# Kernel optimization log

Hardware: AMD Instinct MI355X
Metric: run time of the kernel (lower is better)

The kernel has to match this reference:

```python
import jax, jax.numpy as jnp
import numpy as np

D_MODEL = 1024
NUM_HEADS = 16
D_K = D_MODEL // NUM_HEADS
B, S = 2, 2048


def setup_inputs() -> dict:
    key = jax.random.key(0)
    ks = jax.random.split(key, 11)
    sc = 1.0 / np.sqrt(D_MODEL)
    return {
        "Q_input": jax.random.normal(ks[0], (B, S, D_MODEL), jnp.float32),
        "K_input": jax.random.normal(ks[1], (B, S, D_MODEL), jnp.float32),
        "V_input": jax.random.normal(ks[2], (B, S, D_MODEL), jnp.float32),
        "Wq": jax.random.normal(ks[3], (D_MODEL, D_MODEL), jnp.float32) * sc,
        "bq": jax.random.normal(ks[4], (D_MODEL,), jnp.float32) * 0.01,
        "Wk": jax.random.normal(ks[5], (D_MODEL, D_MODEL), jnp.float32) * sc,
        "bk": jax.random.normal(ks[6], (D_MODEL,), jnp.float32) * 0.01,
        "Wv": jax.random.normal(ks[7], (D_MODEL, D_MODEL), jnp.float32) * sc,
        "bv": jax.random.normal(ks[8], (D_MODEL,), jnp.float32) * 0.01,
        "Wo": jax.random.normal(ks[9], (D_MODEL, D_MODEL), jnp.float32) * sc,
        "bo": jax.random.normal(ks[10], (D_MODEL,), jnp.float32) * 0.01,
    }


def reference(Q_input, K_input, V_input, Wq, bq, Wk, bk, Wv, bv, Wo, bo):
    # Linear projections (torch Linear: x @ W.T + b)
    Q = Q_input @ Wq.T + bq  # [B,S,D]
    K = K_input @ Wk.T + bk
    V = V_input @ Wv.T + bv
    # split heads -> [B,H,S,dk]
    def split(x):
        return x.reshape(B, S, NUM_HEADS, D_K).transpose(0, 2, 1, 3)
    Qh, Kh, Vh = split(Q), split(K), split(V)
    scale = 1.0 / jnp.sqrt(jnp.asarray(D_K, Qh.dtype))
    scores = jnp.einsum('bhqd,bhkd->bhqk', Qh, Kh) * scale  # [B,H,S,S]
    attn = jax.nn.softmax(scores, axis=-1)
    ctx = jnp.einsum('bhqk,bhkd->bhqd', attn, Vh)  # [B,H,S,dk]
    concat = ctx.transpose(0, 2, 1, 3).reshape(B, S, D_MODEL)
    out = concat @ Wo.T + bo  # dropout is identity in eval
    return out
```

## Files before the change

kernel.cpp:

```cpp
#include <hip/hip_runtime.h>
#include <stdint.h>

#define DM   1024
#define NH   16
#define DKH  64
#define BBATCH 2
#define SEQ  2048
#define MTOK (BBATCH*SEQ)

typedef unsigned short u16;
typedef unsigned int   u32;
typedef __attribute__((ext_vector_type(8))) short  bf16x8;
typedef __attribute__((ext_vector_type(4))) float  f32x4;

struct PtrArr11 { const void* p[11]; };
struct U16Arr11 { u16* p[11]; };

__device__ __forceinline__ float bf2f(u16 u) {
  union { unsigned int i; float f; } z; z.i = ((unsigned int)u) << 16; return z.f;
}
__device__ __forceinline__ u16 f2bf(float f) {
  union { float f; unsigned int i; } z; z.f = f;
  unsigned int i = z.i + 0x7fffu + ((z.i >> 16) & 1u);
  return (u16)(i >> 16);
}

__device__ __forceinline__ bf16x8 u4_to_bf(u32 a, u32 b, u32 c, u32 d) {
  union { u32 u[4]; bf16x8 v; } z; z.u[0] = a; z.u[1] = b; z.u[2] = c; z.u[3] = d; return z.v;
}

__device__ __forceinline__ void gld16(const void* g, void* l) {
  __builtin_amdgcn_global_load_lds(
      (const __attribute__((address_space(1))) void*)g,
      (__attribute__((address_space(3))) void*)l,
      16, 0, 0);
}

__global__ void k_detect(const unsigned int* __restrict__ w, int* __restrict__ flag) {
  const int ln = threadIdx.x & 63;
  const unsigned int word = w[ln];
  const unsigned int ex = (word >> 7) & 0xFFu;
  const int hit = (ex >= 100u && ex <= 126u) ? 1 : 0;
  unsigned long long m = __ballot(hit);
  if (ln == 0) *flag = (__popcll(m) >= 40) ? 0 : 1;
}

__global__ __launch_bounds__(256) void k_convert_all(PtrArr11 src, U16Arr11 dst,
                                                     const int* __restrict__ flag) {
  if (*flag == 0) return;
  const int b = blockIdx.x;
  int seg, base;
  if      (b <  2048) { seg = 0;  base = 0;    }
  else if (b <  4096) { seg = 1;  base = 2048; }
  else if (b <  6144) { seg = 2;  base = 4096; }
  else if (b <  6656) { seg = 3;  base = 6144; }
  else if (b == 6656) { seg = 4;  base = 6656; }
  else if (b <  7169) { seg = 5;  base = 6657; }
  else if (b == 7169) { seg = 6;  base = 7169; }
  else if (b <  7682) { seg = 7;  base = 7170; }
  else if (b == 7682) { seg = 8;  base = 7682; }
  else if (b <  8195) { seg = 9;  base = 7683; }
  else                { seg = 10; base = 8195; }
  const int n = (seg < 3) ? (MTOK * DM) : ((seg & 1) ? (DM * DM) : DM);
  const int i0 = (b - base) * 2048 + threadIdx.x * 8;
  if (i0 >= n) return;
  const float* s = (const float*)src.p[seg] + i0;
  const f32x4 x0 = *(const f32x4*)(s);
  const f32x4 x1 = *(const f32x4*)(s + 4);
  bf16x8 o;
#pragma unroll
  for (int j = 0; j < 4; ++j) o[j] = (short)f2bf(x0[j]);
#pragma unroll
  for (int j = 0; j < 4; ++j) o[4 + j] = (short)f2bf(x1[j]);
  *(bf16x8*)(dst.p[seg] + i0) = o;
}

__device__ __forceinline__ void gemm_body64(const u16* __restrict__ X,
                                            const u16* __restrict__ W,
                                            const u16* __restrict__ bias,
                                            void* __restrict__ out,
                                            int isf32out)
{
  __shared__ __attribute__((aligned(16))) u16 sA[128 * 64];
  __shared__ __attribute__((aligned(16))) u16 sB[128 * 64];
  const int tid = threadIdx.x;
  const int ln = tid & 63, wv = tid >> 6;
  const int wm = wv & 1, wn = wv >> 1;
  const int m0 = blockIdx.y * 128, n0 = blockIdx.x * 128;
  const int fr = ln & 15, fq = ln >> 4;
  const int fr7 = fr & 7;
  const int srow = ln >> 3;
  const int scol = ((ln & 7) ^ srow) * 8;

  f32x4 acc[4][4];
#pragma unroll
  for (int i = 0; i < 4; ++i)
#pragma unroll
    for (int j = 0; j < 4; ++j) acc[i][j] = (f32x4){0.f, 0.f, 0.f, 0.f};

  const u16* pA = X + (size_t)(m0 + wv * 32 + srow) * DM + scol;
  const u16* pB = W + (size_t)(n0 + wv * 32 + srow) * DM + scol;
  u16* lA = sA + wv * 32 * 64;
  u16* lB = sB + wv * 32 * 64;

  for (int k0 = 0; k0 < DM; k0 += 64) {
#pragma unroll
    for (int c = 0; c < 4; ++c) {
      gld16(pA + (size_t)(c * 8) * DM + k0, lA + c * 8 * 64);
      gld16(pB + (size_t)(c * 8) * DM + k0, lB + c * 8 * 64);
    }
    asm volatile("s_waitcnt vmcnt(0)" ::: "memory");
    __syncthreads();

    bf16x8 af[4][2], bfg[4][2];
#pragma unroll
    for (int t = 0; t < 4; ++t)
#pragma unroll
      for (int ks = 0; ks < 2; ++ks) {
        af[t][ks]  = *(const bf16x8*)(sA + (wm * 64 + t * 16 + fr) * 64 + ((ks * 4 + fq) ^ fr7) * 8);
        bfg[t][ks] = *(const bf16x8*)(sB + (wn * 64 + t * 16 + fr) * 64 + ((ks * 4 + fq) ^ fr7) * 8);
      }
#pragma unroll
    for (int i = 0; i < 4; ++i)
#pragma unroll
      for (int j = 0; j < 4; ++j) {
        acc[i][j] = __builtin_amdgcn_mfma_f32_16x16x32_bf16(af[i][0], bfg[j][0], acc[i][j], 0, 0, 0);
        acc[i][j] = __builtin_amdgcn_mfma_f32_16x16x32_bf16(af[i][1], bfg[j][1], acc[i][j], 0, 0, 0);
      }
    __syncthreads();
  }

#pragma unroll
  for (int i = 0; i < 4; ++i) {
    const int row = m0 + wm * 64 + i * 16 + fq * 4;
#pragma unroll
    for (int j = 0; j < 4; ++j) {
      const int col = n0 + wn * 64 + j * 16 + fr;
      const float bv = bf2f(bias[col]);
#pragma unroll
      for (int r = 0; r < 4; ++r) {
        const float val = acc[i][j][r] + bv;
        const size_t idx = (size_t)(row + r) * DM + col;
        if (isf32out) ((float*)out)[idx] = val;
        else          ((u16*)out)[idx]   = f2bf(val);
      }
    }
  }
}

__device__ __forceinline__ void gemm_body_n64(const u16* __restrict__ X,
                                              const u16* __restrict__ W,
                                              const u16* __restrict__ bias,
                                              void* __restrict__ out,
                                              int isf32out)
{
  __shared__ __attribute__((aligned(16))) u16 sA[128 * 32];
  __shared__ __attribute__((aligned(16))) u16 sB[64 * 32];
  const int tid = threadIdx.x;
  const int ln = tid & 63, wv = tid >> 6;
  const int wm = wv >> 1, wn = wv & 1;
  const int m0 = blockIdx.y * 128, n0 = blockIdx.x * 64;
  const int fr = ln & 15, fq = ln >> 4;
  const int srow = ln >> 2, sslot = (ln & 3) * 8;

  f32x4 acc[4][2];
#pragma unroll
  for (int i = 0; i < 4; ++i)
#pragma unroll
    for (int j = 0; j < 2; ++j) acc[i][j] = (f32x4){0.f, 0.f, 0.f, 0.f};

  const u16* pA = X + (size_t)(m0 + wv * 32 + srow) * DM + sslot;
  const u16* pB = W + (size_t)(n0 + wv * 16 + srow) * DM + sslot;
  u16* lA0 = sA + (wv * 2) * 512; u16* lA1 = sA + (wv * 2 + 1) * 512;
  u16* lB  = sB + wv * 512;

  for (int k0 = 0; k0 < DM; k0 += 32) {
    gld16(pA + k0,           lA0);
    gld16(pA + 16 * DM + k0, lA1);
    gld16(pB + k0,           lB);
    asm volatile("s_waitcnt vmcnt(0)" ::: "memory");
    __syncthreads();

    bf16x8 af[4], bfg[2];
#pragma unroll
    for (int t = 0; t < 4; ++t)
      af[t]  = *(const bf16x8*)(sA + (wm * 64 + t * 16 + fr) * 32 + fq * 8);
#pragma unroll
    for (int t = 0; t < 2; ++t)
      bfg[t] = *(const bf16x8*)(sB + (wn * 32 + t * 16 + fr) * 32 + fq * 8);
#pragma unroll
    for (int i = 0; i < 4; ++i)
#pragma unroll
      for (int j = 0; j < 2; ++j)
        acc[i][j] = __builtin_amdgcn_mfma_f32_16x16x32_bf16(af[i], bfg[j], acc[i][j], 0, 0, 0);
    __syncthreads();
  }

#pragma unroll
  for (int i = 0; i < 4; ++i) {
    const int row = m0 + wm * 64 + i * 16 + fq * 4;
#pragma unroll
    for (int j = 0; j < 2; ++j) {
      const int col = n0 + wn * 32 + j * 16 + fr;
      const float bv = bf2f(bias[col]);
#pragma unroll
      for (int r = 0; r < 4; ++r) {
        const float val = acc[i][j][r] + bv;
        const size_t idx = (size_t)(row + r) * DM + col;
        if (isf32out) ((float*)out)[idx] = val;
        else          ((u16*)out)[idx]   = f2bf(val);
      }
    }
  }
}

__global__ __launch_bounds__(256, 2) void k_gemm_qkv(
    PtrArr11 orig, U16Arr11 conv, const int* __restrict__ flag,
    u16* oq, u16* ok, u16* ov)
{
  const int f = *flag;
  const int z = blockIdx.z;
  const u16* X  = f ? conv.p[z]         : (const u16*)orig.p[z];
  const u16* W  = f ? conv.p[3 + 2 * z] : (const u16*)orig.p[3 + 2 * z];
  const u16* bi = f ? conv.p[4 + 2 * z] : (const u16*)orig.p[4 + 2 * z];
  u16* o = (z == 0) ? oq : (z == 1) ? ok : ov;
  gemm_body64(X, W, bi, o, 0);
}

__global__ __launch_bounds__(256, 2) void k_gemm_one(
    const u16* X, const void* Wo_o, const u16* Wo_c,
    const void* bo_o, const u16* bo_c, const int* __restrict__ flag, void* o)
{
  const int f = *flag;
  const u16* W  = f ? Wo_c : (const u16*)Wo_o;
  const u16* bi = f ? bo_c : (const u16*)bo_o;
  gemm_body_n64(X, W, bi, o, f);
}

__global__ __launch_bounds__(256) void k_transpose(const u16* __restrict__ in,
                                                   u16* __restrict__ out)
{
  __shared__ u16 t[64][66];
  const int b = blockIdx.z;
  const int s0 = blockIdx.x * 64, d0 = blockIdx.y * 64;
  const int c = threadIdx.x & 63, r0 = threadIdx.x >> 6;
#pragma unroll
  for (int i = 0; i < 16; ++i) {
    const int r = r0 + 4 * i;
    t[r][c] = in[(size_t)(b * SEQ + s0 + r) * DM + d0 + c];
  }
  __syncthreads();
#pragma unroll
  for (int i = 0; i < 16; ++i) {
    const int r = r0 + 4 * i;
    out[(size_t)(b * DM + d0 + r) * SEQ + s0 + c] = t[c][r];
  }
}

__global__ __launch_bounds__(256, 2) void k_attn(
    const u16* __restrict__ Qp, const u16* __restrict__ Kp,
    const u16* __restrict__ Vt, u16* __restrict__ ctx)
{
  __shared__ __attribute__((aligned(16))) u16 sK[2][64 * 64];
  __shared__ __attribute__((aligned(16))) u16 sV[2][64 * 64];

  const int tid = threadIdx.x;
  const int ln = tid & 63, wv = tid >> 6;
  const int bh = blockIdx.y;
  const int b = bh >> 4, h = bh & 15;
  const int q0 = blockIdx.x * 128 + wv * 32;
  const int fr = ln & 15, fq = ln >> 4;
  const int fr7 = fr & 7;

  const int srow = ln >> 3;
  const int scol = ((ln & 7) ^ srow) * 8;
  const u16* gK0 = Kp + (size_t)(b * SEQ + wv * 16 + srow) * DM + h * DKH + scol;
  const u16* gV0 = Vt + (size_t)(b * DM + h * DKH + wv * 16 + srow) * SEQ + scol;
  u16* sKb = &sK[0][0];
  u16* sVb = &sV[0][0];

  bf16x8 qf[2][2];
#pragma unroll
  for (int qt = 0; qt < 2; ++qt)
#pragma unroll
    for (int ks = 0; ks < 2; ++ks) {
      const u16* src = Qp + (size_t)(b * SEQ + q0 + qt * 16 + fr) * DM + h * DKH + ks * 32 + fq * 8;
      bf16x8 v = *(const bf16x8*)src;
      bf16x8 w;
#pragma unroll
      for (int j = 0; j < 8; ++j) w[j] = (short)f2bf(bf2f((u16)v[j]) * 0.125f);
      qf[qt][ks] = w;
    }

  float l_a[2] = {0.f, 0.f};
  float l_b[2] = {0.f, 0.f};
  f32x4 o_acc[2][4];
#pragma unroll
  for (int qt = 0; qt < 2; ++qt)
#pragma unroll
    for (int dt = 0; dt < 4; ++dt) o_acc[qt][dt] = (f32x4){0.f, 0.f, 0.f, 0.f};

#define STAGE_KV(pp, key0)                                     \
  do {                                                         \
    u16* kd = sKb + (pp) * 4096 + wv * 1024;                   \
    u16* vd = sVb + (pp) * 4096 + wv * 1024;                   \
    gld16(gK0 + (size_t)(key0) * DM, kd);                      \
    gld16(gK0 + (size_t)((key0) + 8) * DM, kd + 512);          \
    gld16(gV0 + (key0), vd);                                   \
    gld16(gV0 + (key0) + 8 * SEQ, vd + 512);                   \
  } while (0)

  STAGE_KV(0, 0);
  asm volatile("s_waitcnt vmcnt(0)" ::: "memory");
  __syncthreads();

  int p = 0;
  for (int kb = 0; kb < SEQ / 64; ++kb) {
    if (kb + 1 < SEQ / 64) STAGE_KV(p ^ 1, (kb + 1) * 64);

    const u16* K = sKb + p * 4096;
    const u16* V = sVb + p * 4096;

    bf16x8 kf[4][2];
#pragma unroll
    for (int nt = 0; nt < 4; ++nt)
#pragma unroll
      for (int ks = 0; ks < 2; ++ks)
        kf[nt][ks] = *(const bf16x8*)(K + (nt * 16 + fr) * 64 + ((ks * 4 + fq) ^ fr7) * 8);

    u32 pw[2][2][4];
#pragma unroll
    for (int qt = 0; qt < 2; ++qt) {
      f32x4 s_acc[4];
#pragma unroll
      for (int nt = 0; nt < 4; ++nt) s_acc[nt] = (f32x4){0.f, 0.f, 0.f, 0.f};
      __builtin_amdgcn_s_setprio(1);
#pragma unroll
      for (int nt = 0; nt < 4; ++nt)
#pragma unroll
        for (int ks = 0; ks < 2; ++ks)
          s_acc[nt] = __builtin_amdgcn_mfma_f32_16x16x32_bf16(kf[nt][ks], qf[qt][ks], s_acc[nt], 0, 0, 0);
      __builtin_amdgcn_s_setprio(0);

      u32 w[4][2];
#pragma unroll
      for (int nt = 0; nt < 4; ++nt)
#pragma unroll
        for (int t = 0; t < 2; ++t) {
          const float e0 = __expf(s_acc[nt][2 * t]);
          const float e1 = __expf(s_acc[nt][2 * t + 1]);
          l_a[qt] += e0;
          l_b[qt] += e1;
          u32 wd;
          asm("v_cvt_pk_bf16_f32 %0, %1, %2" : "=v"(wd) : "v"(e0), "v"(e1));
          w[nt][t] = wd;
        }
#pragma unroll
      for (int ks = 0; ks < 2; ++ks) {
        u32 a0 = w[2 * ks][0], b0 = w[2 * ks + 1][0];
        u32 a1 = w[2 * ks][1], b1 = w[2 * ks + 1][1];
        asm("v_permlane32_swap_b32 %0, %1" : "+v"(a0), "+v"(b0));
        asm("v_permlane16_swap_b32 %0, %1" : "+v"(a0), "+v"(b0));
        asm("v_permlane32_swap_b32 %0, %1" : "+v"(a1), "+v"(b1));
        asm("v_permlane16_swap_b32 %0, %1" : "+v"(a1), "+v"(b1));
        pw[qt][ks][0] = a0; pw[qt][ks][1] = a1; pw[qt][ks][2] = b0; pw[qt][ks][3] = b1;
      }
    }

#pragma unroll
    for (int dt = 0; dt < 4; ++dt) {
      bf16x8 vf0 = *(const bf16x8*)(V + (dt * 16 + fr) * 64 + ((0 + fq) ^ fr7) * 8);
      bf16x8 vf1 = *(const bf16x8*)(V + (dt * 16 + fr) * 64 + ((4 + fq) ^ fr7) * 8);
      __builtin_amdgcn_s_setprio(1);
#pragma unroll
      for (int qt = 0; qt < 2; ++qt) {
        o_acc[qt][dt] = __builtin_amdgcn_mfma_f32_16x16x32_bf16(
            u4_to_bf(pw[qt][0][0], pw[qt][0][1], pw[qt][0][2], pw[qt][0][3]), vf0, o_acc[qt][dt], 0, 0, 0);
        o_acc[qt][dt] = __builtin_amdgcn_mfma_f32_16x16x32_bf16(
            u4_to_bf(pw[qt][1][0], pw[qt][1][1], pw[qt][1][2], pw[qt][1][3]), vf1, o_acc[qt][dt], 0, 0, 0);
      }
      __builtin_amdgcn_s_setprio(0);
    }

    asm volatile("s_waitcnt vmcnt(0)" ::: "memory");
    __syncthreads();
    p ^= 1;
  }
#undef STAGE_KV

  float iv[2][4];
#pragma unroll
  for (int qt = 0; qt < 2; ++qt) {
    float t = l_a[qt] + l_b[qt];
    t += __shfl_xor(t, 16);
    t += __shfl_xor(t, 32);
    const float rl = 1.0f / t;
#pragma unroll
    for (int rr = 0; rr < 4; ++rr) iv[qt][rr] = __shfl(rl, fq * 4 + rr);
  }
#pragma unroll
  for (int qt = 0; qt < 2; ++qt)
#pragma unroll
    for (int dt = 0; dt < 4; ++dt)
#pragma unroll
      for (int r = 0; r < 4; ++r) {
        const int qrow = q0 + qt * 16 + fq * 4 + r;
        const int col = h * DKH + dt * 16 + fr;
        ctx[(size_t)(b * SEQ + qrow) * DM + col] = f2bf(o_acc[qt][dt][r] * iv[qt][r]);
      }
}

extern "C" void kernel_launch(void* const* d_in, const int* in_sizes, int n_in,
                              void* d_out, int out_size, void* d_ws, size_t ws_size,
                              hipStream_t stream)
{
  char* ws = (char*)d_ws;
  int* flag = (int*)ws;

  const size_t TOKSZ = (size_t)MTOK * DM * sizeof(u16);
  const size_t WSZ   = (size_t)DM * DM * sizeof(u16);
  const size_t BSZ   = 4096;

  size_t off = 256;
  u16* Qc  = (u16*)(ws + off); off += TOKSZ;
  u16* Kc  = (u16*)(ws + off); off += TOKSZ;
  u16* Vc  = (u16*)(ws + off); off += TOKSZ;
  u16* Wqc = (u16*)(ws + off); off += WSZ;
  u16* Wkc = (u16*)(ws + off); off += WSZ;
  u16* Wvc = (u16*)(ws + off); off += WSZ;
  u16* Woc = (u16*)(ws + off); off += WSZ;
  u16* bqc = (u16*)(ws + off); off += BSZ;
  u16* bkc = (u16*)(ws + off); off += BSZ;
  u16* bvc = (u16*)(ws + off); off += BSZ;
  u16* boc = (u16*)(ws + off); off += BSZ;
  u16* Qp  = (u16*)(ws + off); off += TOKSZ;
  u16* Kp  = (u16*)(ws + off); off += TOKSZ;
  u16* Vp  = (u16*)(ws + off); off += TOKSZ;
  u16* Vt  = Qc;
  u16* ctx = Kc;

  PtrArr11 orig;
  for (int i = 0; i < 11; ++i) orig.p[i] = d_in[i];
  U16Arr11 conv;
  conv.p[0] = Qc;  conv.p[1] = Kc;  conv.p[2] = Vc;
  conv.p[3] = Wqc; conv.p[4] = bqc; conv.p[5] = Wkc; conv.p[6] = bkc;
  conv.p[7] = Wvc; conv.p[8] = bvc; conv.p[9] = Woc; conv.p[10] = boc;

  dim3 blk(256);

  k_detect<<<1, 64, 0, stream>>>((const unsigned int*)d_in[3], flag);
  k_convert_all<<<8196, blk, 0, stream>>>(orig, conv, flag);
  k_gemm_qkv<<<dim3(DM / 128, MTOK / 128, 3), blk, 0, stream>>>(
      orig, conv, flag, Qp, Kp, Vp);
  k_transpose<<<dim3(SEQ / 64, DM / 64, BBATCH), blk, 0, stream>>>(Vp, Vt);
  k_attn<<<dim3(SEQ / 128, BBATCH * NH), blk, 0, stream>>>(Qp, Kp, Vt, ctx);
  k_gemm_one<<<dim3(DM / 64, MTOK / 128, 1), blk, 0, stream>>>(
      ctx, d_in[9], Woc, d_in[10], boc, flag, d_out);
}
```

Measured before the change: 235.5 us.

## Fuse fp32-to-bf16 activation conversion into QKV GEMM A-tile loads

The separate conversion pass over the three fp32 activation tensors is removed. The QKV GEMM now reads fp32 activations directly, converts them with packed bf16 conversion instructions, and stores them to LDS, so only the weights still go through the conversion kernel. This saves a full write and read of the converted activations, but the A-tile load moves from asynchronous global-to-LDS copies to register-staged loads. The attention kernel also remaps block indices so that neighbouring blocks cover groups of heads, probably for better cache locality of K and V.

Result: slower. 248.6 us (+5.6%).

```diff
diff --git a/kernel.cpp b/kernel.cpp
--- a/kernel.cpp
+++ b/kernel.cpp
@@ -45,23 +45,20 @@
   if (ln == 0) *flag = (__popcll(m) >= 40) ? 0 : 1;
 }
 
-__global__ __launch_bounds__(256) void k_convert_all(PtrArr11 src, U16Arr11 dst,
-                                                     const int* __restrict__ flag) {
+__global__ __launch_bounds__(256) void k_convert_w(PtrArr11 src, U16Arr11 dst,
+                                                   const int* __restrict__ flag) {
   if (*flag == 0) return;
   const int b = blockIdx.x;
   int seg, base;
-  if      (b <  2048) { seg = 0;  base = 0;    }
-  else if (b <  4096) { seg = 1;  base = 2048; }
-  else if (b <  6144) { seg = 2;  base = 4096; }
-  else if (b <  6656) { seg = 3;  base = 6144; }
-  else if (b == 6656) { seg = 4;  base = 6656; }
-  else if (b <  7169) { seg = 5;  base = 6657; }
-  else if (b == 7169) { seg = 6;  base = 7169; }
-  else if (b <  7682) { seg = 7;  base = 7170; }
-  else if (b == 7682) { seg = 8;  base = 7682; }
-  else if (b <  8195) { seg = 9;  base = 7683; }
-  else                { seg = 10; base = 8195; }
-  const int n = (seg < 3) ? (MTOK * DM) : ((seg & 1) ? (DM * DM) : DM);
+  if      (b <  512)  { seg = 3;  base = 0;    }
+  else if (b == 512)  { seg = 4;  base = 512;  }
+  else if (b <  1025) { seg = 5;  base = 513;  }
+  else if (b == 1025) { seg = 6;  base = 1025; }
+  else if (b <  1538) { seg = 7;  base = 1026; }
+  else if (b == 1538) { seg = 8;  base = 1538; }
+  else if (b <  2051) { seg = 9;  base = 1539; }
+  else                { seg = 10; base = 2051; }
+  const int n = (seg & 1) ? (DM * DM) : DM;
   const int i0 = (b - base) * 2048 + threadIdx.x * 8;
   if (i0 >= n) return;
   const float* s = (const float*)src.p[seg] + i0;
@@ -75,11 +72,10 @@
   *(bf16x8*)(dst.p[seg] + i0) = o;
 }
 
-__device__ __forceinline__ void gemm_body64(const u16* __restrict__ X,
+__device__ __forceinline__ void gemm_body64(const void* __restrict__ Xv, int xf32,
                                             const u16* __restrict__ W,
                                             const u16* __restrict__ bias,
-                                            void* __restrict__ out,
-                                            int isf32out)
+                                            u16* __restrict__ out)
 {
   __shared__ __attribute__((aligned(16))) u16 sA[128 * 64];
   __shared__ __attribute__((aligned(16))) u16 sB[128 * 64];
@@ -98,17 +94,35 @@
 #pragma unroll
     for (int j = 0; j < 4; ++j) acc[i][j] = (f32x4){0.f, 0.f, 0.f, 0.f};
 
-  const u16* pA = X + (size_t)(m0 + wv * 32 + srow) * DM + scol;
+  const u16*  pA16 = (const u16*)Xv  + (size_t)(m0 + wv * 32 + srow) * DM + scol;
+  const float* pA32 = (const float*)Xv + (size_t)(m0 + wv * 32 + srow) * DM + scol;
   const u16* pB = W + (size_t)(n0 + wv * 32 + srow) * DM + scol;
   u16* lA = sA + wv * 32 * 64;
   u16* lB = sB + wv * 32 * 64;
+  const int lane8 = ln * 8;
 
   for (int k0 = 0; k0 < DM; k0 += 64) {
-#pragma unroll
-    for (int c = 0; c < 4; ++c) {
-      gld16(pA + (size_t)(c * 8) * DM + k0, lA + c * 8 * 64);
-      gld16(pB + (size_t)(c * 8) * DM + k0, lB + c * 8 * 64);
-    }
+    if (xf32) {
+#pragma unroll
+      for (int c = 0; c < 4; ++c) {
+        const float* s = pA32 + (size_t)(c * 8) * DM + k0;
+        const f32x4 x0 = *(const f32x4*)s;
+        const f32x4 x1 = *(const f32x4*)(s + 4);
+        u32 w0, w1, w2, w3;
+        asm("v_cvt_pk_bf16_f32 %0, %1, %2" : "=v"(w0) : "v"(x0[0]), "v"(x0[1]));
+        asm("v_cvt_pk_bf16_f32 %0, %1, %2" : "=v"(w1) : "v"(x0[2]), "v"(x0[3]));
+        asm("v_cvt_pk_bf16_f32 %0, %1, %2" : "=v"(w2) : "v"(x1[0]), "v"(x1[1]));
+        asm("v_cvt_pk_bf16_f32 %0, %1, %2" : "=v"(w3) : "v"(x1[2]), "v"(x1[3]));
+        *(bf16x8*)(lA + c * 512 + lane8) = u4_to_bf(w0, w1, w2, w3);
+      }
+    } else {
+#pragma unroll
+      for (int c = 0; c < 4; ++c)
+        gld16(pA16 + (size_t)(c * 8) * DM + k0, lA + c * 512);
+    }
+#pragma unroll
+    for (int c = 0; c < 4; ++c)
+      gld16(pB + (size_t)(c * 8) * DM + k0, lB + c * 512);
     asm volatile("s_waitcnt vmcnt(0)" ::: "memory");
     __syncthreads();
 
@@ -138,12 +152,8 @@
       const int col = n0 + wn * 64 + j * 16 + fr;
       const float bv = bf2f(bias[col]);
 #pragma unroll
-      for (int r = 0; r < 4; ++r) {
-        const float val = acc[i][j][r] + bv;
-        const size_t idx = (size_t)(row + r) * DM + col;
-        if (isf32out) ((float*)out)[idx] = val;
-        else          ((u16*)out)[idx]   = f2bf(val);
-      }
+      for (int r = 0; r < 4; ++r)
+        out[(size_t)(row + r) * DM + col] = f2bf(acc[i][j][r] + bv);
     }
   }
 }
@@ -220,11 +230,11 @@
 {
   const int f = *flag;
   const int z = blockIdx.z;
-  const u16* X  = f ? conv.p[z]         : (const u16*)orig.p[z];
+  const void* X = orig.p[z];
   const u16* W  = f ? conv.p[3 + 2 * z] : (const u16*)orig.p[3 + 2 * z];
   const u16* bi = f ? conv.p[4 + 2 * z] : (const u16*)orig.p[4 + 2 * z];
   u16* o = (z == 0) ? oq : (z == 1) ? ok : ov;
-  gemm_body64(X, W, bi, o, 0);
+  gemm_body64(X, f, W, bi, o);
 }
 
 __global__ __launch_bounds__(256, 2) void k_gemm_one(
@@ -266,9 +276,12 @@
 
   const int tid = threadIdx.x;
   const int ln = tid & 63, wv = tid >> 6;
-  const int bh = blockIdx.y;
+  const int bid = blockIdx.y * 16 + blockIdx.x;
+  const int kk  = bid >> 3;
+  const int bh  = ((kk >> 4) << 3) | (bid & 7);
+  const int qx  = kk & 15;
   const int b = bh >> 4, h = bh & 15;
-  const int q0 = blockIdx.x * 128 + wv * 32;
+  const int q0 = qx * 128 + wv * 32;
   const int fr = ln & 15, fq = ln >> 4;
   const int fr7 = fr & 7;
 
@@ -449,7 +462,7 @@
   dim3 blk(256);
 
   k_detect<<<1, 64, 0, stream>>>((const unsigned int*)d_in[3], flag);
-  k_convert_all<<<8196, blk, 0, stream>>>(orig, conv, flag);
+  k_convert_w<<<2052, blk, 0, stream>>>(orig, conv, flag);
   k_gemm_qkv<<<dim3(DM / 128, MTOK / 128, 3), blk, 0, stream>>>(
       orig, conv, flag, Qp, Kp, Vp);
   k_transpose<<<dim3(SEQ / 64, DM / 64, BBATCH), blk, 0, stream>>>(Vp, Vt);
```
